# Optimization experiments

Measured on AMD Instinct MI355X. Metric: run time of the kernel, lower is better.

The kernel has to match this reference:

```python
import jax, jax.numpy as jnp
import numpy as np

NEG_BIG = -9e15  # matches -9000000000000000.0 in the torch source
ALPHA = 0.2      # LeakyReLU negative slope


def setup_inputs() -> dict:
    key = jax.random.key(0)
    k1, k2, k3, k4 = jax.random.split(key, 4)
    N, F_in, F_out = 8192, 256, 128
    x = jax.random.normal(k1, (N, F_in), dtype=jnp.float32)
    adj = jax.random.randint(k2, (N, N), 0, 2, dtype=jnp.int32)
    W = jax.random.normal(k3, (F_in, F_out), dtype=jnp.float32) * 0.05
    a = jax.random.normal(k4, (2 * F_out, 1), dtype=jnp.float32) * 0.05
    return {"x": x, "adj": adj, "W": W, "a": a}


def reference(x, adj, W, a):
    # h = x @ W : [N, F]
    h = x @ W
    F_out = W.shape[1]
    # Algebraically identical to the concat formulation:
    # a^T [h_i || h_j] = h_i @ a1 + h_j @ a2
    a1 = a[:F_out, 0]
    a2 = a[F_out:, 0]
    src = h @ a1  # [N]
    dst = h @ a2  # [N]
    e = jax.nn.leaky_relu(src[:, None] + dst[None, :], negative_slope=ALPHA)  # [N, N]
    attention = jnp.where(adj > 0, e, NEG_BIG)
    attention = jax.nn.softmax(attention, axis=1)
    # dropout is identity in eval mode (training=False)
    h_prime = attention @ h  # [N, F]
    return h_prime
```

## Files before the change

### kernel.cpp

```cpp
#include <hip/hip_runtime.h>
#include <cstdint>

#define N 8192
#define FIN 256
#define FOUT 128
#define ALPHA 0.2f
#define JP 4
#define JSL (N / JP)
#define TJ 64
#define NTILE (JSL / TJ)
#define RB 32
#define SST 72

typedef unsigned short u16;
typedef unsigned char u8;
typedef __attribute__((ext_vector_type(8))) short short8;
typedef __attribute__((ext_vector_type(4))) float floatx4;

__device__ __forceinline__ u16 bf16_rne(float f) {
  uint32_t u = __float_as_uint(f);
  u += 0x7fff + ((u >> 16) & 1);
  return (u16)(u >> 16);
}

__device__ __forceinline__ void gl_lds16(const void* g, void* l) {
  __builtin_amdgcn_global_load_lds(
      (const __attribute__((address_space(1))) void*)g,
      (__attribute__((address_space(3))) void*)l, 16, 0, 0);
}

__global__ __launch_bounds__(256) void k_pack(const int* __restrict__ adj,
                                              uint32_t* __restrict__ bm) {
  const int t = blockIdx.x * 256 + threadIdx.x;
  const int4* p = (const int4*)adj + (size_t)t * 8;
  int4 v[8];
  #pragma unroll
  for (int k = 0; k < 8; ++k) v[k] = p[k];
  uint32_t m = 0;
  #pragma unroll
  for (int k = 0; k < 8; ++k) {
    m |= (uint32_t)(v[k].x > 0) << (4 * k + 0);
    m |= (uint32_t)(v[k].y > 0) << (4 * k + 1);
    m |= (uint32_t)(v[k].z > 0) << (4 * k + 2);
    m |= (uint32_t)(v[k].w > 0) << (4 * k + 3);
  }
  bm[t] = m;
}

__global__ __launch_bounds__(256) void k_proj(const float* __restrict__ x,
                                              const float* __restrict__ W,
                                              const float* __restrict__ a,
                                              u16* __restrict__ hT3,
                                              float* __restrict__ srcv,
                                              float* __restrict__ dstv) {
  __shared__ float xs[8 * FIN];
  __shared__ float partS[4][4], partD[4][4];
  const int t = threadIdx.x;
  const int R0 = blockIdx.x * 8;

  const float4* xv = (const float4*)(x + (size_t)R0 * FIN);
  float4* xsv = (float4*)xs;
  xsv[t] = xv[t];
  xsv[t + 256] = xv[t + 256];
  __syncthreads();

  const int c  = t & 127;
  const int rg = (t >> 7) * 4;

  float acc[4] = {0.f, 0.f, 0.f, 0.f};
  float wa[4], wb[4];
  #pragma unroll
  for (int j = 0; j < 4; ++j) wa[j] = W[j * FOUT + c];
  #pragma unroll
  for (int j = 0; j < 4; ++j) wb[j] = W[(4 + j) * FOUT + c];

  for (int k4 = 0; k4 < FIN / 4; ++k4) {
    float wc[4];
    #pragma unroll
    for (int j = 0; j < 4; ++j) { wc[j] = wa[j]; wa[j] = wb[j]; }
    const int kn = (k4 + 2 < FIN / 4) ? k4 + 2 : k4;
    #pragma unroll
    for (int j = 0; j < 4; ++j) wb[j] = W[(kn * 4 + j) * FOUT + c];
    #pragma unroll
    for (int i = 0; i < 4; ++i) {
      const float4 xq = *(const float4*)&xs[(rg + i) * FIN + k4 * 4];
      acc[i] += xq.x * wc[0] + xq.y * wc[1] + xq.z * wc[2] + xq.w * wc[3];
    }
  }

  {
    const int j = R0 + rg;
    const int jb = j >> 5, q = (j >> 3) & 3, jj = j & 7;
    const int m = c & 15, nt = c >> 4;
    union { u16 u[4]; uint2 v; } pk;
    #pragma unroll
    for (int i = 0; i < 4; ++i) pk.u[i] = bf16_rne(acc[i]);
    *(uint2*)(hT3 + (size_t)(((jb * 8 + nt) * 64) + (m * 4 + q)) * 8 + jj) = pk.v;
  }

  const float a1 = a[c], a2 = a[FOUT + c];
  float s4[4], d4[4];
  #pragma unroll
  for (int i = 0; i < 4; ++i) { s4[i] = acc[i] * a1; d4[i] = acc[i] * a2; }
  #pragma unroll
  for (int off = 32; off > 0; off >>= 1) {
    #pragma unroll
    for (int i = 0; i < 4; ++i) {
      s4[i] += __shfl_down(s4[i], off);
      d4[i] += __shfl_down(d4[i], off);
    }
  }
  const int wv = t >> 6, lane = t & 63;
  if (lane == 0) {
    #pragma unroll
    for (int i = 0; i < 4; ++i) { partS[wv][i] = s4[i]; partD[wv][i] = d4[i]; }
  }
  __syncthreads();
  if (t < 16) {
    const int i = t & 3, rg2 = (t >> 2) & 1, which = t >> 3;
    if (which == 0) srcv[R0 + rg2 * 4 + i] = partS[rg2*2][i] + partS[rg2*2+1][i];
    else            dstv[R0 + rg2 * 4 + i] = partD[rg2*2][i] + partD[rg2*2+1][i];
  }
}

__global__ __launch_bounds__(256, 4) void k_gat(const u8* __restrict__ bmk,
                                                const u16* __restrict__ hT3,
                                                const float* __restrict__ srcv,
                                                const float* __restrict__ dstv,
                                                float* __restrict__ P,
                                                float* __restrict__ lp) {
  __shared__ u16 hS[2][8192];
  __shared__ u16 S[RB * SST];
  const int t = threadIdx.x;
  const int wv = t >> 6, lane = t & 63;
  const int q = lane >> 4, m = lane & 15;
  const int bm = blockIdx.x & 255;
  const int jp = blockIdx.x >> 8;
  const int R0 = bm * RB;
  const int j0 = jp * JSL;

  const int pr = t >> 3;
  const int pc = (t & 7) * 8;
  const float srcr = srcv[R0 + pr];
  const u8*    bmp  = bmk + (size_t)(R0 + pr) * (N / 8) + (j0 + pc) / 8;
  const float* dstp = dstv + j0 + pc;

  const int rh = wv & 1, ch = wv >> 1;
  const int Lq = m * 4 + q;

  floatx4 acc[4];
  #pragma unroll
  for (int nt = 0; nt < 4; ++nt) acc[nt] = (floatx4){0.f, 0.f, 0.f, 0.f};
  float lsum = 0.f;

  const size_t jb00 = (size_t)(j0 >> 5);
  #define STAGE(I, BUF)                                                        \
  {                                                                            \
    _Pragma("unroll")                                                          \
    for (int cc = 0; cc < 4; ++cc) {                                           \
      const int kc = wv * 4 + cc;                                   \
      const int jbl = kc >> 3, nt_ = kc & 7;                                   \
      const u16* src = hT3 + ((jb00 + (size_t)(I) * 2 + jbl) * 8 + nt_) * 512  \
                       + (size_t)lane * 8;                                     \
      gl_lds16(src, &hS[BUF][kc * 512]);                                       \
    }                                                                          \
  }

  STAGE(0, 0)
  __builtin_amdgcn_sched_barrier(0);
  u8     aC  = bmp[0];
  float4 dC0 = *(const float4*)(dstp),   dC1 = *(const float4*)(dstp + 4);

  int buf = 0;
  for (int i = 0; i < NTILE; ++i) {
    asm volatile("s_waitcnt vmcnt(3) lgkmcnt(0)" ::: "memory");
    __builtin_amdgcn_s_barrier();
    __builtin_amdgcn_sched_barrier(0);

    const int nx = (i + 1 < NTILE) ? i + 1 : i;
    if (i + 1 < NTILE) STAGE(i + 1, buf ^ 1)
    __builtin_amdgcn_sched_barrier(0);
    u8     aN  = bmp[nx * 8];
    float4 dN0 = *(const float4*)(dstp + nx * TJ);
    float4 dN1 = *(const float4*)(dstp + nx * TJ + 4);

    {
      const float df[8] = {dC0.x, dC0.y, dC0.z, dC0.w, dC1.x, dC1.y, dC1.z, dC1.w};
      union { u16 u[8]; short8 s; } pk;
      #pragma unroll
      for (int e = 0; e < 8; ++e) {
        float v = srcr + df[e];
        v = fmaxf(v, ALPHA * v);
        const float p = ((aC >> e) & 1) ? __expf(v) : 0.f;
        lsum += p;
        pk.u[e] = bf16_rne(p);
      }
      *(short8*)&S[pr * SST + pc] = pk.s;
    }

    asm volatile("s_waitcnt lgkmcnt(0)" ::: "memory");
    __builtin_amdgcn_s_barrier();
    __builtin_amdgcn_sched_barrier(0);

    {
      const short8 a0 = *(const short8*)&S[(rh * 16 + m) * SST + q * 8];
      const short8 a1 = *(const short8*)&S[(rh * 16 + m) * SST + 32 + q * 8];
      #pragma unroll
      for (int nt = 0; nt < 4; ++nt) {
        const short8 b0 = *(const short8*)&hS[buf][(0 * 8 + ch * 4 + nt) * 512 + Lq * 8];
        const short8 b1 = *(const short8*)&hS[buf][(1 * 8 + ch * 4 + nt) * 512 + Lq * 8];
        acc[nt] = __builtin_amdgcn_mfma_f32_16x16x32_bf16(a0, b0, acc[nt], 0, 0, 0);
        acc[nt] = __builtin_amdgcn_mfma_f32_16x16x32_bf16(a1, b1, acc[nt], 0, 0, 0);
      }
    }

    aC = aN; dC0 = dN0; dC1 = dN1;
    buf ^= 1;
  }
  #undef STAGE

  lsum += __shfl_down(lsum, 4);
  lsum += __shfl_down(lsum, 2);
  lsum += __shfl_down(lsum, 1);
  if ((t & 7) == 0) lp[(size_t)jp * N + R0 + pr] = lsum;

  float* Pp = P + ((size_t)jp * N + R0 + rh * 16) * FOUT + ch * 64;
  #pragma unroll
  for (int nt = 0; nt < 4; ++nt)
    #pragma unroll
    for (int ri = 0; ri < 4; ++ri)
      Pp[(size_t)(q * 4 + ri) * FOUT + nt * 16 + m] = acc[nt][ri];
}

__global__ __launch_bounds__(256) void k_norm(const float* __restrict__ P,
                                              const float* __restrict__ lp,
                                              float* __restrict__ out) {
  const int idx = blockIdx.x * 256 + threadIdx.x;
  const int rr = idx >> 5;
  const int c4 = (idx & 31) * 4;
  float l = 0.f;
  #pragma unroll
  for (int j = 0; j < JP; ++j) l += lp[j * N + rr];
  const float inv = 1.0f / l;
  float4 s = {0.f, 0.f, 0.f, 0.f};
  #pragma unroll
  for (int j = 0; j < JP; ++j) {
    const float4 p = *(const float4*)(P + ((size_t)j * N + rr) * FOUT + c4);
    s.x += p.x; s.y += p.y; s.z += p.z; s.w += p.w;
  }
  s.x *= inv; s.y *= inv; s.z *= inv; s.w *= inv;
  *(float4*)(out + (size_t)rr * FOUT + c4) = s;
}

extern "C" void kernel_launch(void* const* d_in, const int* in_sizes, int n_in,
                              void* d_out, int out_size, void* d_ws, size_t ws_size,
                              hipStream_t stream) {
  const float* x   = (const float*)d_in[0];
  const int*   adj = (const int*)d_in[1];
  const float* W   = (const float*)d_in[2];
  const float* a   = (const float*)d_in[3];
  float* out = (float*)d_out;

  char* ws = (char*)d_ws;
  u16*   hT3  = (u16*)ws;     ws += (size_t)FOUT * N * sizeof(u16);
  float* srcv = (float*)ws;   ws += (size_t)N * sizeof(float);
  float* dstv = (float*)ws;   ws += (size_t)N * sizeof(float);
  float* P    = (float*)ws;   ws += (size_t)JP * N * FOUT * sizeof(float);
  float* lp   = (float*)ws;   ws += (size_t)JP * N * sizeof(float);
  u8*    bmk  = (u8*)ws;      ws += (size_t)N * (N / 8);

  k_pack<<<(N / 32) * (N / 256), 256, 0, stream>>>(adj, (uint32_t*)bmk);
  k_proj<<<N / 8, 256, 0, stream>>>(x, W, a, hT3, srcv, dstv);
  k_gat <<<256 * JP, 256, 0, stream>>>(bmk, hT3, srcv, dstv, P, lp);
  k_norm<<<(N * FOUT / 4) / 256, 256, 0, stream>>>(P, lp, out);
}
```

Baseline: 435.8 us.

## Drop LDS staging in attention kernel; compute probability fragments per wave in registers

The attention-times-h kernel no longer stages h tiles into LDS with global_load_lds, and no longer passes the exponentiated scores through a shared S buffer guarded by barriers. Each wave now loads its own B fragments for its two column tiles straight from global memory into registers, double-buffered by software across tiles. Each wave also builds the full 32x64 A fragments itself (mask, leaky ReLU, exp, bf16 pack). This removes the per-tile block barriers and the LDS round-trips, at the cost of four times as many exp and mask operations and more register pressure. The launch-bounds occupancy hint is also dropped.

```diff
diff --git a/kernel.cpp b/kernel.cpp
--- a/kernel.cpp
+++ b/kernel.cpp
@@ -10,7 +10,6 @@
 #define TJ 64
 #define NTILE (JSL / TJ)
 #define RB 32
-#define SST 72
 
 typedef unsigned short u16;
 typedef unsigned char u8;
@@ -21,12 +20,6 @@
   uint32_t u = __float_as_uint(f);
   u += 0x7fff + ((u >> 16) & 1);
   return (u16)(u >> 16);
-}
-
-__device__ __forceinline__ void gl_lds16(const void* g, void* l) {
-  __builtin_amdgcn_global_load_lds(
-      (const __attribute__((address_space(1))) void*)g,
-      (__attribute__((address_space(3))) void*)l, 16, 0, 0);
 }
 
 __global__ __launch_bounds__(256) void k_pack(const int* __restrict__ adj,
@@ -123,113 +116,118 @@
   }
 }
 
-__global__ __launch_bounds__(256, 4) void k_gat(const u8* __restrict__ bmk,
-                                                const u16* __restrict__ hT3,
-                                                const float* __restrict__ srcv,
-                                                const float* __restrict__ dstv,
-                                                float* __restrict__ P,
-                                                float* __restrict__ lp) {
-  __shared__ u16 hS[2][8192];
-  __shared__ u16 S[RB * SST];
+__global__ __launch_bounds__(256) void k_gat(const u8* __restrict__ bmk,
+                                             const u16* __restrict__ hT3,
+                                             const float* __restrict__ srcv,
+                                             const float* __restrict__ dstv,
+                                             float* __restrict__ P,
+                                             float* __restrict__ lp) {
   const int t = threadIdx.x;
-  const int wv = t >> 6, lane = t & 63;
+  const int w = t >> 6, lane = t & 63;
   const int q = lane >> 4, m = lane & 15;
   const int bm = blockIdx.x & 255;
   const int jp = blockIdx.x >> 8;
   const int R0 = bm * RB;
   const int j0 = jp * JSL;
-
-  const int pr = t >> 3;
-  const int pc = (t & 7) * 8;
-  const float srcr = srcv[R0 + pr];
-  const u8*    bmp  = bmk + (size_t)(R0 + pr) * (N / 8) + (j0 + pc) / 8;
-  const float* dstp = dstv + j0 + pc;
-
-  const int rh = wv & 1, ch = wv >> 1;
+  const int nt0 = 2 * w, nt1 = 2 * w + 1;
   const int Lq = m * 4 + q;
 
-  floatx4 acc[4];
-  #pragma unroll
-  for (int nt = 0; nt < 4; ++nt) acc[nt] = (floatx4){0.f, 0.f, 0.f, 0.f};
-  float lsum = 0.f;
+  const float sr0 = srcv[R0 + m];
+  const float sr1 = srcv[R0 + 16 + m];
+  const float* dstp = dstv + j0 + q * 8;
+  const u8* bmp0 = bmk + (size_t)(R0 + m) * (N >> 3) + (j0 >> 3) + q;
+  const u8* bmp1 = bmp0 + (size_t)16 * (N >> 3);
 
   const size_t jb00 = (size_t)(j0 >> 5);
-  #define STAGE(I, BUF)                                                        \
+  const u16* b00 = hT3 + ((jb00 + 0) * 8 + nt0) * 512 + Lq * 8;
+  const u16* b01 = hT3 + ((jb00 + 0) * 8 + nt1) * 512 + Lq * 8;
+  const u16* b10 = hT3 + ((jb00 + 1) * 8 + nt0) * 512 + Lq * 8;
+  const u16* b11 = hT3 + ((jb00 + 1) * 8 + nt1) * 512 + Lq * 8;
+
+  floatx4 acc[2][2];
+  #pragma unroll
+  for (int i = 0; i < 2; ++i)
+    #pragma unroll
+    for (int j = 0; j < 2; ++j) acc[i][j] = (floatx4){0.f, 0.f, 0.f, 0.f};
+  float ls0 = 0.f, ls1 = 0.f;
+
+  auto mk_frag = [&](float srcr, const float4 dlo, const float4 dhi,
+                     const u8 mk, float& ls) -> short8 {
+    union { u16 u[8]; short8 s; } A_;
+    const float df[8] = {dlo.x, dlo.y, dlo.z, dlo.w, dhi.x, dhi.y, dhi.z, dhi.w};
+    #pragma unroll
+    for (int e = 0; e < 8; ++e) {
+      float v = srcr + df[e];
+      v = fmaxf(v, ALPHA * v);
+      const float p = ((mk >> e) & 1) ? __expf(v) : 0.f;
+      ls += p;
+      A_.u[e] = bf16_rne(p);
+    }
+    return A_.s;
+  };
+
+  #define LOADT(T, B00, B01, B10, B11, D0, D1, D2, D3, M00, M01, M10, M11)     \
+    B00 = *(const short8*)(b00 + (size_t)(T) * 8192);                          \
+    B01 = *(const short8*)(b01 + (size_t)(T) * 8192);                          \
+    B10 = *(const short8*)(b10 + (size_t)(T) * 8192);                          \
+    B11 = *(const short8*)(b11 + (size_t)(T) * 8192);                          \
+    D0 = *(const float4*)(dstp + (T) * TJ);                                    \
+    D1 = *(const float4*)(dstp + (T) * TJ + 4);                                \
+    D2 = *(const float4*)(dstp + (T) * TJ + 32);                               \
+    D3 = *(const float4*)(dstp + (T) * TJ + 36);                               \
+    M00 = bmp0[(T) * 8]; M01 = bmp0[(T) * 8 + 4];                              \
+    M10 = bmp1[(T) * 8]; M11 = bmp1[(T) * 8 + 4];
+
+  #define COMPT(B00, B01, B10, B11, D0, D1, D2, D3, M00, M01, M10, M11)        \
   {                                                                            \
-    _Pragma("unroll")                                                          \
-    for (int cc = 0; cc < 4; ++cc) {                                           \
-      const int kc = wv * 4 + cc;                                   \
-      const int jbl = kc >> 3, nt_ = kc & 7;                                   \
-      const u16* src = hT3 + ((jb00 + (size_t)(I) * 2 + jbl) * 8 + nt_) * 512  \
-                       + (size_t)lane * 8;                                     \
-      gl_lds16(src, &hS[BUF][kc * 512]);                                       \
-    }                                                                          \
-  }
-
-  STAGE(0, 0)
-  __builtin_amdgcn_sched_barrier(0);
-  u8     aC  = bmp[0];
-  float4 dC0 = *(const float4*)(dstp),   dC1 = *(const float4*)(dstp + 4);
-
-  int buf = 0;
-  for (int i = 0; i < NTILE; ++i) {
-    asm volatile("s_waitcnt vmcnt(3) lgkmcnt(0)" ::: "memory");
-    __builtin_amdgcn_s_barrier();
-    __builtin_amdgcn_sched_barrier(0);
-
-    const int nx = (i + 1 < NTILE) ? i + 1 : i;
-    if (i + 1 < NTILE) STAGE(i + 1, buf ^ 1)
-    __builtin_amdgcn_sched_barrier(0);
-    u8     aN  = bmp[nx * 8];
-    float4 dN0 = *(const float4*)(dstp + nx * TJ);
-    float4 dN1 = *(const float4*)(dstp + nx * TJ + 4);
-
-    {
-      const float df[8] = {dC0.x, dC0.y, dC0.z, dC0.w, dC1.x, dC1.y, dC1.z, dC1.w};
-      union { u16 u[8]; short8 s; } pk;
+    const short8 a00 = mk_frag(sr0, D0, D1, M00, ls0);            \
+    const short8 a01 = mk_frag(sr0, D2, D3, M01, ls0);            \
+    const short8 a10 = mk_frag(sr1, D0, D1, M10, ls1);            \
+    const short8 a11 = mk_frag(sr1, D2, D3, M11, ls1);            \
+    acc[0][0] = __builtin_amdgcn_mfma_f32_16x16x32_bf16(a00, B00, acc[0][0], 0, 0, 0); \
+    acc[0][0] = __builtin_amdgcn_mfma_f32_16x16x32_bf16(a01, B10, acc[0][0], 0, 0, 0); \
+    acc[0][1] = __builtin_amdgcn_mfma_f32_16x16x32_bf16(a00, B01, acc[0][1], 0, 0, 0); \
+    acc[0][1] = __builtin_amdgcn_mfma_f32_16x16x32_bf16(a01, B11, acc[0][1], 0, 0, 0); \
+    acc[1][0] = __builtin_amdgcn_mfma_f32_16x16x32_bf16(a10, B00, acc[1][0], 0, 0, 0); \
+    acc[1][0] = __builtin_amdgcn_mfma_f32_16x16x32_bf16(a11, B10, acc[1][0], 0, 0, 0); \
+    acc[1][1] = __builtin_amdgcn_mfma_f32_16x16x32_bf16(a10, B01, acc[1][1], 0, 0, 0); \
+    acc[1][1] = __builtin_amdgcn_mfma_f32_16x16x32_bf16(a11, B11, acc[1][1], 0, 0, 0); \
+  }
+
+  short8 cB00, cB01, cB10, cB11, nB00, nB01, nB10, nB11;
+  float4 cD0, cD1, cD2, cD3, nD0, nD1, nD2, nD3;
+  u8 cM00, cM01, cM10, cM11, nM00, nM01, nM10, nM11;
+
+  LOADT(0, cB00, cB01, cB10, cB11, cD0, cD1, cD2, cD3, cM00, cM01, cM10, cM11)
+  for (int i = 0; i < NTILE; i += 2) {
+    const int t1 = (i + 1 < NTILE) ? i + 1 : i;
+    LOADT(t1, nB00, nB01, nB10, nB11, nD0, nD1, nD2, nD3, nM00, nM01, nM10, nM11)
+    COMPT(cB00, cB01, cB10, cB11, cD0, cD1, cD2, cD3, cM00, cM01, cM10, cM11)
+    const int t2 = (i + 2 < NTILE) ? i + 2 : i;
+    LOADT(t2, cB00, cB01, cB10, cB11, cD0, cD1, cD2, cD3, cM00, cM01, cM10, cM11)
+    COMPT(nB00, nB01, nB10, nB11, nD0, nD1, nD2, nD3, nM00, nM01, nM10, nM11)
+  }
+  #undef LOADT
+  #undef COMPT
+
+  ls0 += __shfl_xor(ls0, 16);
+  ls0 += __shfl_xor(ls0, 32);
+  ls1 += __shfl_xor(ls1, 16);
+  ls1 += __shfl_xor(ls1, 32);
+  if (w == 0 && q == 0) {
+    lp[(size_t)jp * N + R0 + m] = ls0;
+    lp[(size_t)jp * N + R0 + 16 + m] = ls1;
+  }
+
+  float* Pp = P + ((size_t)jp * N + R0) * FOUT;
+  #pragma unroll
+  for (int rh = 0; rh < 2; ++rh)
+    #pragma unroll
+    for (int n = 0; n < 2; ++n)
       #pragma unroll
-      for (int e = 0; e < 8; ++e) {
-        float v = srcr + df[e];
-        v = fmaxf(v, ALPHA * v);
-        const float p = ((aC >> e) & 1) ? __expf(v) : 0.f;
-        lsum += p;
-        pk.u[e] = bf16_rne(p);
-      }
-      *(short8*)&S[pr * SST + pc] = pk.s;
-    }
-
-    asm volatile("s_waitcnt lgkmcnt(0)" ::: "memory");
-    __builtin_amdgcn_s_barrier();
-    __builtin_amdgcn_sched_barrier(0);
-
-    {
-      const short8 a0 = *(const short8*)&S[(rh * 16 + m) * SST + q * 8];
-      const short8 a1 = *(const short8*)&S[(rh * 16 + m) * SST + 32 + q * 8];
-      #pragma unroll
-      for (int nt = 0; nt < 4; ++nt) {
-        const short8 b0 = *(const short8*)&hS[buf][(0 * 8 + ch * 4 + nt) * 512 + Lq * 8];
-        const short8 b1 = *(const short8*)&hS[buf][(1 * 8 + ch * 4 + nt) * 512 + Lq * 8];
-        acc[nt] = __builtin_amdgcn_mfma_f32_16x16x32_bf16(a0, b0, acc[nt], 0, 0, 0);
-        acc[nt] = __builtin_amdgcn_mfma_f32_16x16x32_bf16(a1, b1, acc[nt], 0, 0, 0);
-      }
-    }
-
-    aC = aN; dC0 = dN0; dC1 = dN1;
-    buf ^= 1;
-  }
-  #undef STAGE
-
-  lsum += __shfl_down(lsum, 4);
-  lsum += __shfl_down(lsum, 2);
-  lsum += __shfl_down(lsum, 1);
-  if ((t & 7) == 0) lp[(size_t)jp * N + R0 + pr] = lsum;
-
-  float* Pp = P + ((size_t)jp * N + R0 + rh * 16) * FOUT + ch * 64;
-  #pragma unroll
-  for (int nt = 0; nt < 4; ++nt)
-    #pragma unroll
-    for (int ri = 0; ri < 4; ++ri)
-      Pp[(size_t)(q * 4 + ri) * FOUT + nt * 16 + m] = acc[nt][ri];
+      for (int ri = 0; ri < 4; ++ri)
+        Pp[(size_t)(rh * 16 + q * 4 + ri) * FOUT + (nt0 + n) * 16 + m] =
+            acc[rh][n][ri];
 }
 
 __global__ __launch_bounds__(256) void k_norm(const float* __restrict__ P,
```

After: 501.6 us. 15.1% more time.
